# Optimization experiments

Measured on AMD Instinct MI355X. Metric: run time of the kernel, lower is better.

The kernel has to match this reference:

```python
import jax, jax.numpy as jnp
import numpy as np

EPS_Q = 1e-4     # ridge added to L L^T in OptNet.forward
MAX_ITER = 20    # qpth pdipm_b maxIter
BIG = 1e10       # sentinel for inactive step-length entries


def _make_kkt_solver(Q, G):
    """Shared factorizations (qpth pre_factor_kkt): Q Cholesky and S0 = G Q^{-1} G^T."""
    nineq = G.shape[0]
    Lq = jnp.linalg.cholesky(Q)                                   # [nz, nz]

    def q_solve(rhs):                                             # rhs [B, nz] -> Q^{-1} rhs
        return jax.scipy.linalg.cho_solve((Lq, True), rhs.T).T

    S0 = G @ jax.scipy.linalg.cho_solve((Lq, True), G.T)          # [nineq, nineq]
    eye = jnp.eye(nineq, dtype=Q.dtype)

    def solve(d, rx, rs, rz):
        # Solve the reduced KKT system (qpth solve_kkt, neq=0):
        #   [Q G^T; G -D^{-1}] [dx; dz] = [-rx; -rz + D^{-1} rs],  ds = (-rs - dz)/d
        invQ_rx = q_solve(rx)                                     # [B, nz]
        hv = invQ_rx @ G.T + rs / d - rz                          # [B, nineq]
        S = S0[None] + eye * (1.0 / d)[:, None, :]                # S0 + diag(1/d) per batch
        dz = -jnp.linalg.solve(S, hv[..., None])[..., 0]
        dx = q_solve(-rx - dz @ G)
        ds = (-rs - dz) / d
        return dx, ds, dz

    return solve


def _get_step(v, dv):
    # max alpha with v + alpha*dv >= 0 (min over entries with dv < 0); safe against NaN grads
    dv_safe = jnp.where(dv < 0, dv, -1.0)
    a = jnp.where(dv < 0, -v / dv_safe, BIG)
    return jnp.min(a, axis=1)


def pdipm_forward(Q, p, G, h):
    """qpth pdipm_b.forward (Mehrotra predictor-corrector), neq=0, fixed 20 iters with best-tracking."""
    nB, nz = p.shape
    nineq = G.shape[0]
    solve = _make_kkt_solver(Q, G)

    # initial point: KKT solve with d = 1, then shift s, z into the positive orthant
    d0 = jnp.ones((nB, nineq), Q.dtype)
    zeros = jnp.zeros((nB, nineq), Q.dtype)
    x, s, z = solve(d0, p, zeros, -h)
    smin = jnp.min(s, axis=1, keepdims=True)
    s = jnp.where(smin < 0, s - smin + 1.0, s)
    zmin = jnp.min(z, axis=1, keepdims=True)
    z = jnp.where(zmin < 0, z - zmin + 1.0, z)

    def body(carry, _):
        x, s, z, bx, bz, bs, bsum = carry
        rx = x @ Q + p + z @ G          # stationarity residual (Q symmetric)
        rs = z
        rz = x @ G.T + s - h            # primal residual
        mu = jnp.abs(jnp.sum(s * z, axis=1)) / nineq
        resids = jnp.linalg.norm(rz, axis=1) + jnp.linalg.norm(rx, axis=1) + nineq * mu
        rsum = jnp.sum(resids)
        imp = rsum < bsum
        bx = jnp.where(imp, x, bx)
        bz = jnp.where(imp, z, bz)
        bs = jnp.where(imp, s, bs)
        bsum = jnp.where(imp, rsum, bsum)
        d = z / s
        # affine (predictor) step
        dx_a, ds_a, dz_a = solve(d, rx, rs, rz)
        alpha = jnp.minimum(jnp.minimum(_get_step(z, dz_a), _get_step(s, ds_a)), 1.0)[:, None]
        sig = (jnp.sum((s + alpha * ds_a) * (z + alpha * dz_a), axis=1)
               / jnp.sum(s * z, axis=1)) ** 3
        # centering + corrector step
        rs_c = ((-mu * sig)[:, None] + ds_a * dz_a) / s
        dx_c, ds_c, dz_c = solve(d, jnp.zeros_like(rx), rs_c, jnp.zeros_like(rz))
        dx = dx_a + dx_c
        ds = ds_a + ds_c
        dz = dz_a + dz_c
        alpha = jnp.minimum(0.999 * jnp.minimum(_get_step(z, dz), _get_step(s, ds)), 1.0)[:, None]
        x = x + alpha * dx
        s = s + alpha * ds
        z = z + alpha * dz
        return (x, s, z, bx, bz, bs, bsum), None

    init = (x, s, z, x, z, s, jnp.asarray(np.inf, dtype=Q.dtype))
    (x, s, z, bx, bz, bs, bsum), _ = jax.lax.scan(body, init, None, length=MAX_ITER)
    return bx, bz, bs                   # zhat, lam (dual), slack


def setup_inputs() -> dict:
    key = jax.random.key(0)
    k1, k2, k3 = jax.random.split(key, 3)
    B, nz, nineq = 128, 512, 512
    x = jax.random.normal(k1, (B, nz), dtype=jnp.float32)
    M = jnp.tril(jnp.ones((nz, nz), jnp.float32))                        # Parameter M = tril(ones)
    L = jnp.tril(jax.random.uniform(k2, (nz, nz), dtype=jnp.float32))    # Parameter L = tril(rand)
    G = jax.random.uniform(k3, (nineq, nz), dtype=jnp.float32, minval=-1.0, maxval=1.0)
    s0 = jnp.ones((nineq,), jnp.float32)
    z0 = jnp.zeros((nz,), jnp.float32)
    return {"x": x, "M": M, "L": L, "G": G, "s0": s0, "z0": z0}


def reference(x, M, L, G, s0, z0):
    nz = L.shape[0]
    Lm = M * L
    Q = Lm @ Lm.T + EPS_Q * jnp.eye(nz, dtype=L.dtype)                   # PSD + ridge
    h = jnp.broadcast_to(z0 @ G.T + s0, (x.shape[0], G.shape[0]))        # h = G z0 + s0
    zhat, _, _ = pdipm_forward(Q, x, G, h)                               # p = x
    return zhat
```

## Files before the change

### kernel.cpp

```cpp
#include <hip/hip_runtime.h>
#include <math.h>

#define BIGD 1e10
#define N2C 262144
#define PITCH_AS 257
#define FACF 131328

typedef double d4 __attribute__((ext_vector_type(4)));

__device__ __forceinline__ int tile_off(int bi, int bj) {
    return 512 * bi * (bi - 1) + 528 * bi + (bj << 10);
}
__device__ __forceinline__ int tile_off_diag(int bi) {
    return 512 * bi * (bi - 1) + 528 * bi + (bi << 10);
}

__device__ __forceinline__ double blk_reduce_sum_d(double v, double* red) {
    int tid = threadIdx.x;
    red[tid] = v; __syncthreads();
    for (int s = 128; s > 0; s >>= 1) {
        if (tid < s) red[tid] += red[tid + s];
        __syncthreads();
    }
    double r = red[0]; __syncthreads();
// ... 88 lines not shown
    for (int l = 0; l < 4; ++l) {
        int y = y0 + 8 * l;
        t[y][x] = A[(size_t)(by * 32 + y) * 512 + bx * 32 + x];
    }
    __syncthreads();
#pragma unroll
    for (int l = 0; l < 4; ++l) {
        int y = y0 + 8 * l;
        B[(size_t)(bx * 32 + y) * 512 + by * 32 + x] = t[x][y];
    }
}

__global__ void k_h_d(const float* __restrict__ G, const float* __restrict__ s0,
                      const float* __restrict__ z0, double* __restrict__ h) {
    __shared__ double red[256];
    int tid = threadIdx.x;
    int j = blockIdx.x * 64 + (tid >> 2);
    int q = tid & 3;
    double a = 0.0;
    for (int k = q * 128; k < q * 128 + 128; ++k)
        a += (double)G[(size_t)j * 512 + k] * (double)z0[k];
    red[tid] = a;
    __syncthreads();
    if (q == 0) h[j] = (double)s0[j] + red[tid] + red[tid + 1] + red[tid + 2] + red[tid + 3];
}

__global__ __launch_bounds__(256) void k_bgemm_d(
    const double* __restrict__ A1, const double* __restrict__ B1,
    double* __restrict__ C, double sgn, double diag_eps)
{
    __shared__ double As[32 * 68];
    __shared__ double Bs[32 * 68];
    int bid = blockIdx.x;
    int mt = bid >> 3, nt = bid & 7;
    int m0 = mt * 64, n0 = nt * 64;
    int tid = threadIdx.x;
    int tx = tid & 15, ty = tid >> 4;
    double acc[4][4] = {};
    for (int k0 = 0; k0 < 512; k0 += 32) {
        __syncthreads();
#pragma unroll
        for (int l = 0; l < 8; ++l) {
            int idx = tid + 256 * l;
            int kk = idx & 31, r = idx >> 5;
            As[kk * 68 + r] = A1[(size_t)(m0 + r) * 512 + k0 + kk];
            int cc = idx & 63, k2 = idx >> 6;
            Bs[k2 * 68 + cc] = B1[(size_t)(k0 + k2) * 512 + n0 + cc];
        }
        __syncthreads();
#pragma unroll
        for (int kk = 0; kk < 32; ++kk) {
            double a4[4], b4[4];
#pragma unroll
            for (int u = 0; u < 4; ++u) a4[u] = As[kk * 68 + tx * 4 + u];
#pragma unroll
            for (int u = 0; u < 4; ++u) b4[u] = Bs[kk * 68 + ty * 4 + u];
#pragma unroll
            for (int ii = 0; ii < 4; ++ii)
#pragma unroll
                for (int jj = 0; jj < 4; ++jj)
                    acc[ii][jj] += a4[ii] * b4[jj];
        }
    }
#pragma unroll
    for (int ii = 0; ii < 4; ++ii) {
        int gm = m0 + tx * 4 + ii;
#pragma unroll
        for (int jj = 0; jj < 4; ++jj) {
            int gn = n0 + ty * 4 + jj;
            double v = sgn * acc[ii][jj];
            if (diag_eps != 0.0 && gm == gn) v += diag_eps;
            C[(size_t)gm * 512 + gn] = v;
        }
    }
}

__global__ __launch_bounds__(256) void k_gemm32(
    const float* __restrict__ A1, const float* __restrict__ B1,
    const float* __restrict__ A2, const float* __restrict__ B2,
    float* __restrict__ C,
    const float* __restrict__ addp, const float* __restrict__ subp,
    const float* __restrict__ rowp, float rowsgn, float sgn)
{
    __shared__ float As[32 * 68];
    __shared__ float Bs[32 * 68];
    int bid = blockIdx.x;
    int mt = bid >> 3, nt = bid & 7;
    int m0 = mt * 64, n0 = nt * 64;
    int tid = threadIdx.x;
    int tx = tid & 15, ty = tid >> 4;
    double acc[4][4] = {};
    for (int prod = 0; prod < 2; ++prod) {
        const float* A = prod ? A2 : A1;
        const float* B = prod ? B2 : B1;
        if (A == nullptr) break;
        for (int k0 = 0; k0 < 512; k0 += 32) {
            __syncthreads();
#pragma unroll
            for (int l = 0; l < 8; ++l) {
                int idx = tid + 256 * l;
                int kk = idx & 31, r = idx >> 5;
                As[kk * 68 + r] = A[(size_t)(m0 + r) * 512 + k0 + kk];
                int cc = idx & 63, k2 = idx >> 6;
                Bs[k2 * 68 + cc] = B[(size_t)(k0 + k2) * 512 + n0 + cc];
            }
            __syncthreads();
#pragma unroll
            for (int kk = 0; kk < 32; ++kk) {
                double a4[4], b4[4];
#pragma unroll
                for (int u = 0; u < 4; ++u) a4[u] = (double)As[kk * 68 + tx * 4 + u];
#pragma unroll
                for (int u = 0; u < 4; ++u) b4[u] = (double)Bs[kk * 68 + ty * 4 + u];
#pragma unroll
                for (int ii = 0; ii < 4; ++ii)
#pragma unroll
                    for (int jj = 0; jj < 4; ++jj)
                        acc[ii][jj] += a4[ii] * b4[jj];
            }
        }
    }
#pragma unroll
    for (int ii = 0; ii < 4; ++ii) {
        int gm = m0 + tx * 4 + ii;
#pragma unroll
        for (int jj = 0; jj < 4; ++jj) {
            int gn = n0 + ty * 4 + jj;
            size_t gi = (size_t)gm * 512 + gn;
            double v = (double)sgn * acc[ii][jj];
            if (addp) v += (double)addp[gi];
            if (subp) v -= (double)subp[gi];
            if (rowp) v += (double)rowsgn * (double)rowp[gn];
            C[gi] = (float)v;
        }
    }
}

__global__ void k_copyadd_d(const double* __restrict__ S, double* __restrict__ F,
                            double dc, int n) {
    int i = blockIdx.x * 256 + threadIdx.x;
    if (i < n) {
        double v = S[i];
        if (dc != 0.0 && (i >> 9) == (i & 511)) v += dc;
        F[i] = v;
    }
}

__global__ __launch_bounds__(512) void k_cpanel_d(double* __restrict__ F, int kp) {
    int c0 = kp * 32, tid = threadIdx.x;
    __shared__ double Dl[32 * 33];
    __shared__ double rdg[32];
    if (tid < 32) {
        int i = tid;
        double d[32];
#pragma unroll
        for (int j = 0; j < 32; ++j) d[j] = F[(size_t)(c0 + i) * 512 + c0 + j];
#pragma unroll
        for (int j = 0; j < 32; ++j) {
            double djj = __shfl(d[j], j);
            djj = (djj > 1e-300) ? djj : 1e-300;
            double sj = sqrt(djj);
            double inv = 1.0 / sj;
            if (i == j) { d[j] = sj; rdg[j] = inv; }
            if (i > j) d[j] *= inv;
            double lij = d[j];
#pragma unroll
            for (int t = j + 1; t < 32; ++t) {
                double ltj = __shfl(d[j], t);
                if (i >= t) d[t] -= lij * ltj;
            }
        }
#pragma unroll
        for (int j = 0; j < 32; ++j) {
            if (j <= i) {
                Dl[i * 33 + j] = d[j];
                F[(size_t)(c0 + i) * 512 + c0 + j] = d[j];
            }
        }
    }
    __syncthreads();
    int r = c0 + 32 + tid;
    if (r < 512) {
        double p[32];
#pragma unroll
        for (int j = 0; j < 32; ++j) p[j] = F[(size_t)r * 512 + c0 + j];
#pragma unroll
        for (int j = 0; j < 32; ++j) {
            double pj = p[j] * rdg[j];
            p[j] = pj;
#pragma unroll
            for (int t = j + 1; t < 32; ++t) p[t] -= pj * Dl[t * 33 + j];
        }
#pragma unroll
        for (int j = 0; j < 32; ++j) F[(size_t)r * 512 + c0 + j] = p[j];
    }
}

__global__ __launch_bounds__(256) void k_syrk_d(double* __restrict__ F, int kp) {
    int c0 = kp * 32;
    int t = blockIdx.x;
    int bi = 0;
    while ((bi + 1) * (bi + 2) / 2 <= t) ++bi;
    int bj = t - bi * (bi + 1) / 2;
    int i0 = c0 + 32 + bi * 64, j0 = c0 + 32 + bj * 64;
    __shared__ double Pa[32 * 68], Pb[32 * 68];
    int tid = threadIdx.x;
#pragma unroll
// ... 160 lines not shown
            for (int m = 0; m < 32; ++m) a += (double)tp[m] * wp[m];
        }
        red[tid] = a;
        __syncthreads();
        if (tid < 32) {
            int i2 = tid;
            double s = 0.0;
#pragma unroll
            for (int k2 = 0; k2 < 16; ++k2) s += red[i2 * 16 + k2];
            double aa = wv[c0 + i2] - s;
            double rdgv = rdgAll[c0 + i2];
            const float* tp = Lb + tile_off_diag(j);
            int basei = (i2 * (i2 + 1)) >> 1;
            float lrow[32];
#pragma unroll
            for (int m = 0; m < 32; ++m) lrow[m] = (m < i2) ? tp[basei + m] : 0.f;
#pragma unroll
            for (int m = 0; m < 32; ++m) {
                double xm = __shfl(aa * rdgv, m);
                if (i2 == m) wv[c0 + i2] = xm;
                if (i2 > m) aa -= (double)lrow[m] * xm;
            }
        }
        __syncthreads();
    }
    for (int j = 15; j >= 0; --j) {
        int c0 = j * 32;
        if (tid < 32) {
            int i2 = tid;
            double aa = wv[c0 + i2];
            double rdgv = rdgAll[c0 + i2];
            const float* tp = Lb + tile_off_diag(j);
            float lcol[32];
#pragma unroll
            for (int m = 0; m < 32; ++m)
                lcol[m] = (m > i2) ? tp[((m * (m + 1)) >> 1) + i2] : 0.f;
#pragma unroll
            for (int m = 31; m >= 0; --m) {
                double xm = __shfl(aa * rdgv, m);
                if (i2 == m) wv[c0 + i2] = xm;
                if (i2 < m) aa -= (double)lcol[m] * xm;
            }
        }
        __syncthreads();
        if (j > 0) {
            int k = tid >> 5, m = tid & 31;
            if (k < j) {
                const float* tp = Lb + tile_off(j, k) + m;
                double sacc = 0.0;
#pragma unroll 8
                for (int i3 = 0; i3 < 32; ++i3) sacc += (double)tp[i3 * 32] * wv[c0 + i3];
                wv[k * 32 + m] -= sacc;
            }
            __syncthreads();
        }
    }
}

__device__ void refine_once(const double* __restrict__ S0d, const double* __restrict__ dvecS,
                            const double* __restrict__ rhsL, double* __restrict__ wv,
                            double* __restrict__ tmpS, double* __restrict__ red,
                            const float* __restrict__ Lb, const double* __restrict__ rdgAll,
                            int tid)
{
    double a = 0.0;
    const double* sp = S0d + tid;
    for (int c = 0; c < 512; ++c) a += sp[(size_t)c * 512] * wv[c];
    double r = rhsL[tid] - a - dvecS[tid] * wv[tid];
    __syncthreads();
    tmpS[tid] = r;
    __syncthreads();
    trsv_packed(Lb, rdgAll, tmpS, red, tid);
    wv[tid] += tmpS[tid];
    __syncthreads();
}

__global__ __launch_bounds__(512) void k_fused(
    const double* __restrict__ S0d,
    float* __restrict__ F0,
    const double* __restrict__ ss, const double* __restrict__ zs,
    const float* __restrict__ hvf,
    const double* __restrict__ mu, const double* __restrict__ szs,
    float* __restrict__ dzv, float* __restrict__ dsv,
    const int* __restrict__ mfok,
    int b0)
{
    const int tid = threadIdx.x;
    const int b = b0 + blockIdx.x;
    float* Lb = F0 + (size_t)blockIdx.x * FACF;
    const size_t gb = (size_t)b * 512;
    const int useM = mfok[0];

    __shared__ double pool[9376];
    __shared__ double Dl[32 * 33];
    __shared__ double rdgS[32];
    __shared__ double rdgAll[512];
    __shared__ double wv[512], rhsL[512], dvecS[512], tmpS[512], redS[512];
    double* As = pool;
    double* Bs = pool + 32 * PITCH_AS;
    double* W  = pool;

    const int tx = tid & 63, ty = tid >> 6;
    const int lane = tid & 63, wid = tid >> 6;
    const int aoff = lane & 15, koff = lane >> 4;

    for (int j = 0; j < 16; ++j) {
        const int c0 = j * 32;
        for (int rbase = c0; rbase < 512; rbase += 256) {
            const int rows = (512 - rbase < 256) ? (512 - rbase) : 256;

            if (useM) {
                const int ntiles = (rows >> 4) << 1;
                d4 uacc[4];
#pragma unroll
                for (int tt = 0; tt < 4; ++tt) uacc[tt] = (d4){0.0, 0.0, 0.0, 0.0};
                for (int k = 0; k < j; ++k) {
                    __syncthreads();
                    {
                        int rl0 = tid >> 3;
                        int kq = (tid & 7) * 4;
                        for (int rr = rl0; rr < rows; rr += 64) {
                            int gr = rbase + rr;
                            const float* tp = Lb + tile_off(gr >> 5, k) + (gr & 31) * 32 + kq;
                            float4 f4 = *(const float4*)tp;
                            As[(kq + 0) * PITCH_AS + rr] = (double)f4.x;
                            As[(kq + 1) * PITCH_AS + rr] = (double)f4.y;
                            As[(kq + 2) * PITCH_AS + rr] = (double)f4.z;
                            As[(kq + 3) * PITCH_AS + rr] = (double)f4.w;
                        }
                    }
                    {
                        const float* tp = Lb + tile_off(j, k);
#pragma unroll
                        for (int l = 0; l < 2; ++l) {
                            int idx = tid + 512 * l;
                            int c = idx >> 5, kk = idx & 31;
                            Bs[kk * 36 + c] = (double)tp[c * 32 + kk];
                        }
                    }
                    __syncthreads();
#pragma unroll
                    for (int tt = 0; tt < 4; ++tt) {
                        int t = wid + (tt << 3);
                        if (t < ntiles) {
                            int s16 = (t >> 1) << 4, hcol = (t & 1) << 4;
                            d4 uv = uacc[tt];
#pragma unroll
                            for (int k4 = 0; k4 < 8; ++k4) {
                                double av = As[(k4 * 4 + koff) * PITCH_AS + s16 + aoff];
                                double bv = Bs[(k4 * 4 + koff) * 36 + hcol + aoff];
                                uv = __builtin_amdgcn_mfma_f64_16x16x4f64(av, bv, uv, 0, 0, 0);
                            }
                            uacc[tt] = uv;
                        }
                    }
                }
                __syncthreads();
#pragma unroll
                for (int tt = 0; tt < 4; ++tt) {
                    int t = wid + (tt << 3);
                    if (t < ntiles) {
                        int s16 = (t >> 1) << 4, hcol = (t & 1) << 4;
#pragma unroll
                        for (int r = 0; r < 4; ++r) {
                            int li, lj;
                            if (useM == 1)      { li = (koff << 2) + r; lj = aoff; }
                            else if (useM == 2) { li = koff + (r << 2); lj = aoff; }
                            else if (useM == 3) { li = aoff; lj = (koff << 2) + r; }
                            else                { li = aoff; lj = koff + (r << 2); }
                            W[(s16 + li) * 33 + hcol + lj] = uacc[tt][r];
                        }
                    }
                }
                __syncthreads();
#pragma unroll
                for (int v = 0; v < 4; ++v) {
                    int cg = c0 + 4 * ty + v;
                    const double* srow = S0d + (size_t)cg * 512 + rbase + tx;
#pragma unroll
                    for (int uu = 0; uu < 4; ++uu) {
                        int rl = tx + 64 * uu;
                        if (rl < rows) {
                            double sv = srow[64 * uu];
                            int rg = rbase + rl;
                            if (rbase == c0 && rg == cg) sv += ss[gb + rg] / zs[gb + rg];
                            W[rl * 33 + 4 * ty + v] = sv - W[rl * 33 + 4 * ty + v];
                        }
                    }
                }
            } else {
                double acc[4][4];
#pragma unroll
                for (int v = 0; v < 4; ++v) {
                    int cg = c0 + 4 * ty + v;
                    const double* srow = S0d + (size_t)cg * 512 + rbase + tx;
#pragma unroll
                    for (int u = 0; u < 4; ++u) {
                        int rl = tx + 64 * u;
                        acc[u][v] = (rl < rows) ? srow[64 * u] : 0.0;
                    }
                }
                if (rbase == c0) {
#pragma unroll
                    for (int u = 0; u < 4; ++u) {
                        int rg = rbase + tx + 64 * u;
#pragma unroll
                        for (int v = 0; v < 4; ++v) {
                            if (rg == c0 + 4 * ty + v) acc[u][v] += ss[gb + rg] / zs[gb + rg];
                        }
                    }
                }
                for (int k = 0; k < j; ++k) {
                    __syncthreads();
                    {
                        int rl0 = tid >> 3;
                        int kq = (tid & 7) * 4;
                        for (int rr = rl0; rr < rows; rr += 64) {
                            int gr = rbase + rr;
                            const float* tp = Lb + tile_off(gr >> 5, k) + (gr & 31) * 32 + kq;
                            float4 f4 = *(const float4*)tp;
                            As[(kq + 0) * PITCH_AS + rr] = (double)f4.x;
                            As[(kq + 1) * PITCH_AS + rr] = (double)f4.y;
                            As[(kq + 2) * PITCH_AS + rr] = (double)f4.z;
                            As[(kq + 3) * PITCH_AS + rr] = (double)f4.w;
                        }
                    }
                    {
                        const float* tp = Lb + tile_off(j, k);
#pragma unroll
                        for (int l = 0; l < 2; ++l) {
                            int idx = tid + 512 * l;
                            int c = idx >> 5, kk = idx & 31;
                            Bs[kk * 36 + c] = (double)tp[c * 32 + kk];
                        }
                    }
                    __syncthreads();
#pragma unroll 8
                    for (int kk = 0; kk < 32; ++kk) {
                        double a4[4], b4[4];
#pragma unroll
                        for (int u = 0; u < 4; ++u) a4[u] = As[kk * PITCH_AS + tx + 64 * u];
#pragma unroll
                        for (int v = 0; v < 4; ++v) b4[v] = Bs[kk * 36 + 4 * ty + v];
#pragma unroll
                        for (int u = 0; u < 4; ++u)
#pragma unroll
                            for (int v = 0; v < 4; ++v)
                                acc[u][v] -= a4[u] * b4[v];
                    }
                }
                __syncthreads();
#pragma unroll
                for (int u = 0; u < 4; ++u) {
                    int rl = tx + 64 * u;
                    if (rl < rows) {
#pragma unroll
                        for (int v = 0; v < 4; ++v)
                            W[rl * 33 + 4 * ty + v] = acc[u][v];
                    }
                }
            }
            __syncthreads();

            int trsm0 = 0;
            if (rbase == c0) {
                trsm0 = 32;
                if (tid < 32) {
                    int i = tid;
                    double d[32];
#pragma unroll
                    for (int m2 = 0; m2 < 32; ++m2) d[m2] = W[i * 33 + m2];
#pragma unroll
                    for (int m2 = 0; m2 < 32; ++m2) {
                        double djj = __shfl(d[m2], m2);
                        djj = (djj > 1e-30) ? djj : 1e-30;
                        double sj = sqrt(djj);
                        double inv = 1.0 / sj;
                        if (i == m2) { d[m2] = sj; rdgS[m2] = inv; rdgAll[c0 + m2] = inv; }
                        if (i > m2) d[m2] *= inv;
                        double lij = d[m2];
#pragma unroll
                        for (int t2 = m2 + 1; t2 < 32; ++t2) {
                            double ltj = __shfl(d[m2], t2);
                            if (i >= t2) d[t2] -= lij * ltj;
                        }
                    }
                    float* tp = Lb + tile_off_diag(j);
                    int basei = (i * (i + 1)) >> 1;
#pragma unroll
                    for (int m2 = 0; m2 < 32; ++m2) {
                        if (m2 <= i) { Dl[i * 33 + m2] = d[m2]; tp[basei + m2] = (float)d[m2]; }
                    }
                }
                __syncthreads();
            }
            {
                int nr = rows - trsm0;
                if (tid < nr) {
                    int rl = trsm0 + tid;
                    int gr = rbase + rl;
                    double x[32];
#pragma unroll
                    for (int m2 = 0; m2 < 32; ++m2) x[m2] = W[rl * 33 + m2];
#pragma unroll
                    for (int m2 = 0; m2 < 32; ++m2) {
                        double xm = x[m2] * rdgS[m2];
                        x[m2] = xm;
#pragma unroll
                        for (int t2 = m2 + 1; t2 < 32; ++t2) x[t2] -= xm * Dl[t2 * 33 + m2];
                    }
                    float* tp = Lb + tile_off(gr >> 5, j) + (gr & 31) * 32;
#pragma unroll
                    for (int m2 = 0; m2 < 32; ++m2) tp[m2] = (float)x[m2];
                }
            }
            __syncthreads();
        }
    }

    double z_t = zs[gb + tid], s_t = ss[gb + tid];
    double dv = s_t / z_t;
    dvecS[tid] = dv;
    double r1 = (double)hvf[gb + tid];
    wv[tid] = r1;
    rhsL[tid] = r1;
    __syncthreads();
    trsv_packed(Lb, rdgAll, wv, redS, tid);
    refine_once(S0d, dvecS, rhsL, wv, tmpS, redS, Lb, rdgAll, tid);

    double dza_t = -wv[tid];
    double dsa_t = -(z_t + dza_t) * dv;
    __syncthreads();

    double az = (dza_t < 0.0) ? (-z_t / dza_t) : BIGD;
    double as = (dsa_t < 0.0) ? (-s_t / dsa_t) : BIGD;
    redS[tid] = fmin(az, as);
    __syncthreads();
    for (int s2 = 256; s2 > 0; s2 >>= 1) {
        if (tid < s2) redS[tid] = fmin(redS[tid], redS[tid + s2]);
        __syncthreads();
    }
    double alpha = fmin(redS[0], 1.0);
    __syncthreads();
    redS[tid] = (s_t + alpha * dsa_t) * (z_t + alpha * dza_t);
    __syncthreads();
    for (int s2 = 256; s2 > 0; s2 >>= 1) {
        if (tid < s2) redS[tid] += redS[tid + s2];
        __syncthreads();
    }
    double d2 = redS[0];
    __syncthreads();
    double ratio = d2 / szs[b];
    double sig = ratio * ratio * ratio;
    double coef = -mu[b] * sig;
    double num = coef + dsa_t * dza_t;
    double rsc_t = num / s_t;
    wv[tid] = num / z_t;
    rhsL[tid] = wv[tid];
    __syncthreads();

    trsv_packed(Lb, rdgAll, wv, redS, tid);
    refine_once(S0d, dvecS, rhsL, wv, tmpS, redS, Lb, rdgAll, tid);

    double dz = dza_t - wv[tid];
    double ds = -(z_t + rsc_t + dz) * dv;
    dzv[gb + tid] = (float)dz;
    dsv[gb + tid] = (float)ds;
}

__global__ __launch_bounds__(256) void k_stats_d(
    const float* __restrict__ rx, const float* __restrict__ rz,
    const double* __restrict__ ssv, const double* __restrict__ zsv,
    double* resid, double* mu, double* szsum)
{
    int b = blockIdx.x, tid = threadIdx.x;
    __shared__ double red[256];
    double s1 = 0, s2 = 0, s3 = 0;
#pragma unroll
    for (int l = 0; l < 2; ++l) {
        size_t gi = (size_t)b * 512 + tid + l * 256;
        double vx = (double)rx[gi]; s1 += vx * vx;
        double vz = (double)rz[gi]; s2 += vz * vz;
        s3 += ssv[gi] * zsv[gi];
    }
    double t1 = blk_reduce_sum_d(s1, red);
    double t2 = blk_reduce_sum_d(s2, red);
    double t3 = blk_reduce_sum_d(s3, red);
    if (tid == 0) {
        resid[b] = sqrt(t2) + sqrt(t1) + fabs(t3);
        mu[b] = fabs(t3) / 512.0;
        szsum[b] = t3;
    }
}

__global__ void k_best_d(const double* __restrict__ resid, double* bsum, double* flag) {
    __shared__ double red[128];
    int tid = threadIdx.x;
    red[tid] = resid[tid];
    __syncthreads();
    for (int s = 64; s > 0; s >>= 1) {
        if (tid < s) red[tid] += red[tid + s];
        __syncthreads();
    }
    if (tid == 0) {
        double rs = red[0];
        if (rs < bsum[0]) { bsum[0] = rs; flag[0] = 1.0; }
        else flag[0] = 0.0;
    }
}

__global__ void k_bestcopy_d(const double* __restrict__ flag, const double* __restrict__ xs,
                             float* __restrict__ bx) {
    if (flag && flag[0] == 0.0) return;
    int i0 = blockIdx.x * 1024 + threadIdx.x;
#pragma unroll
    for (int l = 0; l < 4; ++l) bx[i0 + l * 256] = (float)xs[i0 + l * 256];
}

__global__ __launch_bounds__(256) void k_final_d(
    double* __restrict__ xs, double* __restrict__ ssv, double* __restrict__ zsv,
    const float* __restrict__ dxf, const float* __restrict__ dsf, const float* __restrict__ dzf,
    float* __restrict__ xs32, float* __restrict__ ss32, float* __restrict__ zs32)
{
    int b = blockIdx.x, tid = threadIdx.x;
    __shared__ double red[256];
    double m = BIGD;
#pragma unroll
    for (int l = 0; l < 2; ++l) {
        size_t gi = (size_t)b * 512 + tid + l * 256;
        double z = zsv[gi], dz = (double)dzf[gi];
        double az = (dz < 0.0) ? (-z / dz) : BIGD;
        double s = ssv[gi], ds = (double)dsf[gi];
        double as = (ds < 0.0) ? (-s / ds) : BIGD;
        m = fmin(m, fmin(az, as));
    }
    double am = blk_reduce_min_d(m, red);
    double alpha = fmin(0.999 * am, 1.0);
#pragma unroll
    for (int l = 0; l < 2; ++l) {
        size_t gi = (size_t)b * 512 + tid + l * 256;
        double nx = xs[gi] + alpha * (double)dxf[gi];
        double ns = ssv[gi] + alpha * (double)dsf[gi];
        double nz = zsv[gi] + alpha * (double)dzf[gi];
        xs[gi] = nx; ssv[gi] = ns; zsv[gi] = nz;
        xs32[gi] = (float)nx; ss32[gi] = (float)ns; zs32[gi] = (float)nz;
    }
}

__global__ __launch_bounds__(256) void k_shift_d(double* __restrict__ ssv, double* __restrict__ zsv,
                                                 float* __restrict__ ss32, float* __restrict__ zs32)
// ... 36 lines not shown
    const float* s0  = (const float*)d_in[4];
    const float* z0  = (const float*)d_in[5];
    float* outp = (float*)d_out;

    const size_t N2 = N2C;
    double* base = (double*)d_ws;
    size_t off = 0;
    auto A = [&](size_t n) { double* p = base + off; off += n; return p; };
    double* S0d  = A(N2);
    double* h    = A(512);
    double* resid = A(128); double* mu = A(128); double* szs = A(128);
    double* bsum = A(8); double* flag = A(8);
    double* mfokd = A(8);
    int* mfok = (int*)mfokd;
    double* xs = A(65536); double* ss = A(65536); double* zs = A(65536);
    float* Qf   = (float*)A(131072);
    float* GTf  = (float*)A(131072);
    float* Qif  = (float*)A(131072);
    float* h32  = (float*)A(256);
    float* rxf  = (float*)A(32768);
    float* rzf  = (float*)A(32768);
    float* hvf  = (float*)A(32768);
    float* t1f  = (float*)A(32768);
    float* dzvf = (float*)A(32768);
    float* dsvf = (float*)A(32768);
    float* xs32 = (float*)A(32768);
    float* ss32 = (float*)A(32768);
    float* zs32 = (float*)A(32768);
    float* dxf = hvf;
    float* t2f = t1f;

    double* slab = base + off;
    size_t avail = (ws_size / 8 > off) ? (ws_size / 8 - off) : 0;
    int C = (int)(avail / (FACF / 2));
    if (C > 128) C = 128;
    if (C < 1) C = 1;
    float* F0 = (float*)slab;
    double* Lm64  = slab;
    double* LmT64 = slab + 1 * N2;
    double* Q64   = slab + 2 * N2;
    double* Lq    = slab + 3 * N2;
    double* Qi64  = slab + 4 * N2;
    double* G64   = slab + 5 * N2;
    double* GT64  = slab + 6 * N2;
    double* X64   = slab + 7 * N2;
    double* SfI   = slab + 8 * N2;

    dim3 t256(256), t512(512);
    const float* NPf = nullptr;

    k_mfmatest<<<1, 64, 0, stream>>>(mfok);
    k_lm<<<1024, t256, 0, stream>>>(Mi, Li, Lm64, 262144);
    k_transpose_d<<<256, t256, 0, stream>>>(Lm64, LmT64);
    k_bgemm_d<<<64, t256, 0, stream>>>(Lm64, LmT64, Q64, 1.0, 1e-4);
    k_cast32v<<<1024, t256, 0, stream>>>(Q64, Qf, 262144);
    k_copyadd_d<<<1024, t256, 0, stream>>>(Q64, Lq, 0.0, 262144);
    for (int kp = 0; kp < 16; ++kp) {
        k_cpanel_d<<<1, t512, 0, stream>>>(Lq, kp);
        int Tr = 480 - 32 * kp;
        if (Tr > 0) {
            int T = (Tr + 63) >> 6;
            k_syrk_d<<<T * (T + 1) / 2, t256, 0, stream>>>(Lq, kp);
        }
    }
    k_solve_d<<<512, t256, 0, stream>>>(Lq, NPf, Qi64, nullptr, Qif, nullptr, 0);
    k_cast<<<1024, t256, 0, stream>>>(Gin, G64, 262144);
    k_transpose_d<<<256, t256, 0, stream>>>(G64, GT64);
    k_transpose32<<<256, t256, 0, stream>>>(Gin, GTf);
    k_bgemm_d<<<64, t256, 0, stream>>>(Qi64, GT64, X64, 1.0, 0.0);
    k_bgemm_d<<<64, t256, 0, stream>>>(G64, X64, S0d, 1.0, 0.0);
    k_copyadd_d<<<1024, t256, 0, stream>>>(S0d, SfI, 1.0, 262144);
    for (int kp = 0; kp < 16; ++kp) {
        k_cpanel_d<<<1, t512, 0, stream>>>(SfI, kp);
        int Tr = 480 - 32 * kp;
        if (Tr > 0) {
            int T = (Tr + 63) >> 6;
            k_syrk_d<<<T * (T + 1) / 2, t256, 0, stream>>>(SfI, kp);
        }
    }
    k_h_d<<<8, t256, 0, stream>>>(Gin, s0, z0, h);
    k_cast32v<<<2, t256, 0, stream>>>(h, h32, 512);
    k_initbsum<<<1, 64, 0, stream>>>(bsum);

    k_gemm32<<<16, t256, 0, stream>>>(xin, Qif, NPf, NPf, t1f, NPf, NPf, NPf, 0.f, 1.f);
    k_gemm32<<<16, t256, 0, stream>>>(t1f, GTf, NPf, NPf, hvf, NPf, NPf, h32, 1.f, 1.f);
    k_solve_d<<<128, t256, 0, stream>>>(SfI, hvf, zs, ss, zs32, ss32, 1);
    k_gemm32<<<16, t256, 0, stream>>>(zs32, Gin, NPf, NPf, t1f, xin, NPf, NPf, 0.f, 1.f);
    k_gemm32<<<16, t256, 0, stream>>>(t1f, Qif, NPf, NPf, xs32, NPf, NPf, NPf, 0.f, -1.f);
    k_cast<<<256, t256, 0, stream>>>(xs32, xs, 65536);
    k_shift_d<<<128, t256, 0, stream>>>(ss, zs, ss32, zs32);
    k_bestcopy_d<<<64, t256, 0, stream>>>(nullptr, xs, outp);

    for (int it = 0; it < 20; ++it) {
        k_gemm32<<<16, t256, 0, stream>>>(xs32, Qf, zs32, Gin, rxf, xin, NPf, NPf, 0.f, 1.f);
        k_gemm32<<<16, t256, 0, stream>>>(xs32, GTf, NPf, NPf, rzf, ss32, NPf, h32, -1.f, 1.f);
        k_stats_d<<<128, t256, 0, stream>>>(rxf, rzf, ss, zs, resid, mu, szs);
        k_best_d<<<1, 128, 0, stream>>>(resid, bsum, flag);
        k_bestcopy_d<<<64, t256, 0, stream>>>(flag, xs, outp);
        k_gemm32<<<16, t256, 0, stream>>>(rxf, Qif, NPf, NPf, t1f, NPf, NPf, NPf, 0.f, 1.f);
        k_gemm32<<<16, t256, 0, stream>>>(t1f, GTf, NPf, NPf, hvf, ss32, rzf, NPf, 0.f, 1.f);
        for (int b0 = 0; b0 < 128; b0 += C) {
            int cnt = (128 - b0 < C) ? (128 - b0) : C;
            k_fused<<<cnt, t512, 0, stream>>>(S0d, F0, ss, zs, hvf, mu, szs, dzvf, dsvf,
                                              mfok, b0);
        }
        k_gemm32<<<16, t256, 0, stream>>>(dzvf, Gin, NPf, NPf, t2f, rxf, NPf, NPf, 0.f, 1.f);
        k_gemm32<<<16, t256, 0, stream>>>(t2f, Qif, NPf, NPf, dxf, NPf, NPf, NPf, 0.f, -1.f);
        k_final_d<<<128, t256, 0, stream>>>(xs, ss, zs, dxf, dsvf, dzvf, xs32, ss32, zs32);
    }
}
```

Before: 50.90 ms.

## Persistent fused Cholesky blocks, double-buffered MFMA panel, smaller GEMM tiles

The per-batch fused Cholesky/solve kernel becomes persistent: each block loops over batch items with a grid stride, replacing the multiple host-side chunked launches with one launch. In the MFMA update path, the A operand is read directly from the packed factor in global memory instead of being staged through LDS, and the B tile is double-buffered in LDS, removing one barrier per k-step. The fp32 GEMM kernel uses 32x64 tiles instead of 64x64, launching 32 blocks rather than 16 to spread the work over more compute units. The direct global loads for A may be less coalesced than the staged copy.

```diff
diff --git a/kernel.cpp b/kernel.cpp
--- a/kernel.cpp
+++ b/kernel.cpp
@@ -194,14 +194,14 @@
     const float* __restrict__ addp, const float* __restrict__ subp,
     const float* __restrict__ rowp, float rowsgn, float sgn)
 {
-    __shared__ float As[32 * 68];
+    __shared__ float As[32 * 36];
     __shared__ float Bs[32 * 68];
     int bid = blockIdx.x;
     int mt = bid >> 3, nt = bid & 7;
-    int m0 = mt * 64, n0 = nt * 64;
+    int m0 = mt * 32, n0 = nt * 64;
     int tid = threadIdx.x;
     int tx = tid & 15, ty = tid >> 4;
-    double acc[4][4] = {};
+    double acc[2][4] = {};
     for (int prod = 0; prod < 2; ++prod) {
         const float* A = prod ? A2 : A1;
         const float* B = prod ? B2 : B1;
@@ -209,32 +209,36 @@
         for (int k0 = 0; k0 < 512; k0 += 32) {
             __syncthreads();
 #pragma unroll
+            for (int l = 0; l < 4; ++l) {
+                int idx = tid + 256 * l;
+                int kk = idx & 31, r = idx >> 5;
+                As[kk * 36 + r] = A[(size_t)(m0 + r) * 512 + k0 + kk];
+            }
+#pragma unroll
             for (int l = 0; l < 8; ++l) {
                 int idx = tid + 256 * l;
-                int kk = idx & 31, r = idx >> 5;
-                As[kk * 68 + r] = A[(size_t)(m0 + r) * 512 + k0 + kk];
                 int cc = idx & 63, k2 = idx >> 6;
                 Bs[k2 * 68 + cc] = B[(size_t)(k0 + k2) * 512 + n0 + cc];
             }
             __syncthreads();
 #pragma unroll
             for (int kk = 0; kk < 32; ++kk) {
-                double a4[4], b4[4];
-#pragma unroll
-                for (int u = 0; u < 4; ++u) a4[u] = (double)As[kk * 68 + tx * 4 + u];
+                double a2[2], b4[4];
+#pragma unroll
+                for (int u = 0; u < 2; ++u) a2[u] = (double)As[kk * 36 + tx * 2 + u];
 #pragma unroll
                 for (int u = 0; u < 4; ++u) b4[u] = (double)Bs[kk * 68 + ty * 4 + u];
 #pragma unroll
-                for (int ii = 0; ii < 4; ++ii)
+                for (int ii = 0; ii < 2; ++ii)
 #pragma unroll
                     for (int jj = 0; jj < 4; ++jj)
-                        acc[ii][jj] += a4[ii] * b4[jj];
-            }
-        }
-    }
-#pragma unroll
-    for (int ii = 0; ii < 4; ++ii) {
-        int gm = m0 + tx * 4 + ii;
+                        acc[ii][jj] += a2[ii] * b4[jj];
+            }
+        }
+    }
+#pragma unroll
+    for (int ii = 0; ii < 2; ++ii) {
+        int gm = m0 + tx * 2 + ii;
 #pragma unroll
         for (int jj = 0; jj < 4; ++jj) {
             int gn = n0 + ty * 4 + jj;
@@ -561,13 +565,10 @@
     const float* __restrict__ hvf,
     const double* __restrict__ mu, const double* __restrict__ szs,
     float* __restrict__ dzv, float* __restrict__ dsv,
-    const int* __restrict__ mfok,
-    int b0)
+    const int* __restrict__ mfok)
 {
     const int tid = threadIdx.x;
-    const int b = b0 + blockIdx.x;
     float* Lb = F0 + (size_t)blockIdx.x * FACF;
-    const size_t gb = (size_t)b * 512;
     const int useM = mfok[0];
 
     __shared__ double pool[9376];
@@ -583,268 +584,276 @@
     const int lane = tid & 63, wid = tid >> 6;
     const int aoff = lane & 15, koff = lane >> 4;
 
-    for (int j = 0; j < 16; ++j) {
-        const int c0 = j * 32;
-        for (int rbase = c0; rbase < 512; rbase += 256) {
-            const int rows = (512 - rbase < 256) ? (512 - rbase) : 256;
-
-            if (useM) {
-                const int ntiles = (rows >> 4) << 1;
-                d4 uacc[4];
-#pragma unroll
-                for (int tt = 0; tt < 4; ++tt) uacc[tt] = (d4){0.0, 0.0, 0.0, 0.0};
-                for (int k = 0; k < j; ++k) {
-                    __syncthreads();
-                    {
-                        int rl0 = tid >> 3;
-                        int kq = (tid & 7) * 4;
-                        for (int rr = rl0; rr < rows; rr += 64) {
-                            int gr = rbase + rr;
-                            const float* tp = Lb + tile_off(gr >> 5, k) + (gr & 31) * 32 + kq;
-                            float4 f4 = *(const float4*)tp;
-                            As[(kq + 0) * PITCH_AS + rr] = (double)f4.x;
-                            As[(kq + 1) * PITCH_AS + rr] = (double)f4.y;
-                            As[(kq + 2) * PITCH_AS + rr] = (double)f4.z;
-                            As[(kq + 3) * PITCH_AS + rr] = (double)f4.w;
+    for (int b = blockIdx.x; b < 128; b += gridDim.x) {
+        const size_t gb = (size_t)b * 512;
+        __syncthreads();
+
+        for (int j = 0; j < 16; ++j) {
+            const int c0 = j * 32;
+            for (int rbase = c0; rbase < 512; rbase += 256) {
+                const int rows = (512 - rbase < 256) ? (512 - rbase) : 256;
+
+                if (useM) {
+                    const int ntiles = (rows >> 4) << 1;
+                    d4 uacc[4];
+#pragma unroll
+                    for (int tt = 0; tt < 4; ++tt) uacc[tt] = (d4){0.0, 0.0, 0.0, 0.0};
+                    if (j > 0) {
+                        {
+                            const float* tp = Lb + tile_off(j, 0);
+#pragma unroll
+                            for (int l = 0; l < 2; ++l) {
+                                int idx = tid + 512 * l;
+                                int c = idx >> 5, kk = idx & 31;
+                                pool[kk * 36 + c] = (double)tp[c * 32 + kk];
+                            }
+                        }
+                        __syncthreads();
+                        for (int k = 0; k < j; ++k) {
+                            double* Bcur = pool + (k & 1) * 1152;
+                            if (k + 1 < j) {
+                                const float* tp = Lb + tile_off(j, k + 1);
+                                double* Bnxt = pool + ((k + 1) & 1) * 1152;
+#pragma unroll
+                                for (int l = 0; l < 2; ++l) {
+                                    int idx = tid + 512 * l;
+                                    int c = idx >> 5, kk = idx & 31;
+                                    Bnxt[kk * 36 + c] = (double)tp[c * 32 + kk];
+                                }
+                            }
+#pragma unroll
+                            for (int tt = 0; tt < 4; ++tt) {
+                                int t = wid + (tt << 3);
+                                if (t < ntiles) {
+                                    int s16 = (t >> 1) << 4, hcol = (t & 1) << 4;
+                                    int gr = rbase + s16 + aoff;
+                                    const float* ap = Lb + tile_off(gr >> 5, k)
+                                                      + (gr & 31) * 32 + koff;
+                                    d4 uv = uacc[tt];
+#pragma unroll
+                                    for (int k4 = 0; k4 < 8; ++k4) {
+                                        double av = (double)ap[k4 * 4];
+                                        double bv = Bcur[(k4 * 4 + koff) * 36 + hcol + aoff];
+                                        uv = __builtin_amdgcn_mfma_f64_16x16x4f64(av, bv, uv,
+                                                                                  0, 0, 0);
+                                    }
+                                    uacc[tt] = uv;
+                                }
+                            }
+                            __syncthreads();
                         }
                     }
-                    {
-                        const float* tp = Lb + tile_off(j, k);
-#pragma unroll
-                        for (int l = 0; l < 2; ++l) {
-                            int idx = tid + 512 * l;
-                            int c = idx >> 5, kk = idx & 31;
-                            Bs[kk * 36 + c] = (double)tp[c * 32 + kk];
-                        }
-                    }
-                    __syncthreads();
 #pragma unroll
                     for (int tt = 0; tt < 4; ++tt) {
                         int t = wid + (tt << 3);
                         if (t < ntiles) {
                             int s16 = (t >> 1) << 4, hcol = (t & 1) << 4;
-                            d4 uv = uacc[tt];
-#pragma unroll
-                            for (int k4 = 0; k4 < 8; ++k4) {
-                                double av = As[(k4 * 4 + koff) * PITCH_AS + s16 + aoff];
-                                double bv = Bs[(k4 * 4 + koff) * 36 + hcol + aoff];
-                                uv = __builtin_amdgcn_mfma_f64_16x16x4f64(av, bv, uv, 0, 0, 0);
+#pragma unroll
+                            for (int r = 0; r < 4; ++r) {
+                                int li, lj;
+                                if (useM == 1)      { li = (koff << 2) + r; lj = aoff; }
+                                else if (useM == 2) { li = koff + (r << 2); lj = aoff; }
+                                else if (useM == 3) { li = aoff; lj = (koff << 2) + r; }
+                                else                { li = aoff; lj = koff + (r << 2); }
+                                W[(s16 + li) * 33 + hcol + lj] = uacc[tt][r];
                             }
-                            uacc[tt] = uv;
+                        }
+                    }
+                    __syncthreads();
+#pragma unroll
+                    for (int v = 0; v < 4; ++v) {
+                        int cg = c0 + 4 * ty + v;
+                        const double* srow = S0d + (size_t)cg * 512 + rbase + tx;
+#pragma unroll
+                        for (int uu = 0; uu < 4; ++uu) {
+                            int rl = tx + 64 * uu;
+                            if (rl < rows) {
+                                double sv = srow[64 * uu];
+                                int rg = rbase + rl;
+                                if (rbase == c0 && rg == cg) sv += ss[gb + rg] / zs[gb + rg];
+                                W[rl * 33 + 4 * ty + v] = sv - W[rl * 33 + 4 * ty + v];
+                            }
+                        }
+                    }
+                } else {
+                    double acc[4][4];
+#pragma unroll
+                    for (int v = 0; v < 4; ++v) {
+                        int cg = c0 + 4 * ty + v;
+                        const double* srow = S0d + (size_t)cg * 512 + rbase + tx;
+#pragma unroll
+                        for (int u = 0; u < 4; ++u) {
+                            int rl = tx + 64 * u;
+                            acc[u][v] = (rl < rows) ? srow[64 * u] : 0.0;
+                        }
+                    }
+                    if (rbase == c0) {
+#pragma unroll
+                        for (int u = 0; u < 4; ++u) {
+                            int rg = rbase + tx + 64 * u;
+#pragma unroll
+                            for (int v = 0; v < 4; ++v) {
+                                if (rg == c0 + 4 * ty + v) acc[u][v] += ss[gb + rg] / zs[gb + rg];
+                            }
+                        }
+                    }
+                    for (int k = 0; k < j; ++k) {
+                        __syncthreads();
+                        {
+                            int rl0 = tid >> 3;
+                            int kq = (tid & 7) * 4;
+                            for (int rr = rl0; rr < rows; rr += 64) {
+                                int gr = rbase + rr;
+                                const float* tp = Lb + tile_off(gr >> 5, k) + (gr & 31) * 32 + kq;
+                                float4 f4 = *(const float4*)tp;
+                                As[(kq + 0) * PITCH_AS + rr] = (double)f4.x;
+                                As[(kq + 1) * PITCH_AS + rr] = (double)f4.y;
+                                As[(kq + 2) * PITCH_AS + rr] = (double)f4.z;
+                                As[(kq + 3) * PITCH_AS + rr] = (double)f4.w;
+                            }
+                        }
+                        {
+                            const float* tp = Lb + tile_off(j, k);
+#pragma unroll
+                            for (int l = 0; l < 2; ++l) {
+                                int idx = tid + 512 * l;
+                                int c = idx >> 5, kk = idx & 31;
+                                Bs[kk * 36 + c] = (double)tp[c * 32 + kk];
+                            }
+                        }
+                        __syncthreads();
+#pragma unroll 8
+                        for (int kk = 0; kk < 32; ++kk) {
+                            double a4[4], b4[4];
+#pragma unroll
+                            for (int u = 0; u < 4; ++u) a4[u] = As[kk * PITCH_AS + tx + 64 * u];
+#pragma unroll
+                            for (int v = 0; v < 4; ++v) b4[v] = Bs[kk * 36 + 4 * ty + v];
+#pragma unroll
+                            for (int u = 0; u < 4; ++u)
+#pragma unroll
+                                for (int v = 0; v < 4; ++v)
+                                    acc[u][v] -= a4[u] * b4[v];
+                        }
+                    }
+                    __syncthreads();
+#pragma unroll
+                    for (int u = 0; u < 4; ++u) {
+                        int rl = tx + 64 * u;
+                        if (rl < rows) {
+#pragma unroll
+                            for (int v = 0; v < 4; ++v)
+                                W[rl * 33 + 4 * ty + v] = acc[u][v];
                         }
                     }
                 }
                 __syncthreads();
-#pragma unroll
-                for (int tt = 0; tt < 4; ++tt) {
-                    int t = wid + (tt << 3);
-                    if (t < ntiles) {
-                        int s16 = (t >> 1) << 4, hcol = (t & 1) << 4;
-#pragma unroll
-                        for (int r = 0; r < 4; ++r) {
-                            int li, lj;
-                            if (useM == 1)      { li = (koff << 2) + r; lj = aoff; }
-                            else if (useM == 2) { li = koff + (r << 2); lj = aoff; }
-                            else if (useM == 3) { li = aoff; lj = (koff << 2) + r; }
-                            else                { li = aoff; lj = koff + (r << 2); }
-                            W[(s16 + li) * 33 + hcol + lj] = uacc[tt][r];
-                        }
+
+                int trsm0 = 0;
+                if (rbase == c0) {
+                    trsm0 = 32;
+                    if (tid < 32) {
+                        int i = tid;
+                        double d[32];
+#pragma unroll
+                        for (int m2 = 0; m2 < 32; ++m2) d[m2] = W[i * 33 + m2];
+#pragma unroll
+                        for (int m2 = 0; m2 < 32; ++m2) {
+                            double djj = __shfl(d[m2], m2);
+                            djj = (djj > 1e-30) ? djj : 1e-30;
+                            double sj = sqrt(djj);
+                            double inv = 1.0 / sj;
+                            if (i == m2) { d[m2] = sj; rdgS[m2] = inv; rdgAll[c0 + m2] = inv; }
+                            if (i > m2) d[m2] *= inv;
+                            double lij = d[m2];
+#pragma unroll
+                            for (int t2 = m2 + 1; t2 < 32; ++t2) {
+                                double ltj = __shfl(d[m2], t2);
+                                if (i >= t2) d[t2] -= lij * ltj;
+                            }
+                        }
+                        float* tp = Lb + tile_off_diag(j);
+                        int basei = (i * (i + 1)) >> 1;
+#pragma unroll
+                        for (int m2 = 0; m2 < 32; ++m2) {
+                            if (m2 <= i) { Dl[i * 33 + m2] = d[m2]; tp[basei + m2] = (float)d[m2]; }
+                        }
+                    }
+                    __syncthreads();
+                }
+                {
+                    int nr = rows - trsm0;
+                    if (tid < nr) {
+                        int rl = trsm0 + tid;
+                        int gr = rbase + rl;
+                        double x[32];
+#pragma unroll
+                        for (int m2 = 0; m2 < 32; ++m2) x[m2] = W[rl * 33 + m2];
+#pragma unroll
+                        for (int m2 = 0; m2 < 32; ++m2) {
+                            double xm = x[m2] * rdgS[m2];
+                            x[m2] = xm;
+#pragma unroll
+                            for (int t2 = m2 + 1; t2 < 32; ++t2) x[t2] -= xm * Dl[t2 * 33 + m2];
+                        }
+                        float* tp = Lb + tile_off(gr >> 5, j) + (gr & 31) * 32;
+#pragma unroll
+                        for (int m2 = 0; m2 < 32; ++m2) tp[m2] = (float)x[m2];
                     }
                 }
                 __syncthreads();
-#pragma unroll
-                for (int v = 0; v < 4; ++v) {
-                    int cg = c0 + 4 * ty + v;
-                    const double* srow = S0d + (size_t)cg * 512 + rbase + tx;
-#pragma unroll
-                    for (int uu = 0; uu < 4; ++uu) {
-                        int rl = tx + 64 * uu;
-                        if (rl < rows) {
-                            double sv = srow[64 * uu];
-                            int rg = rbase + rl;
-                            if (rbase == c0 && rg == cg) sv += ss[gb + rg] / zs[gb + rg];
-                            W[rl * 33 + 4 * ty + v] = sv - W[rl * 33 + 4 * ty + v];
-                        }
-                    }
-                }
-            } else {
-                double acc[4][4];
-#pragma unroll
-                for (int v = 0; v < 4; ++v) {
-                    int cg = c0 + 4 * ty + v;
-                    const double* srow = S0d + (size_t)cg * 512 + rbase + tx;
-#pragma unroll
-                    for (int u = 0; u < 4; ++u) {
-                        int rl = tx + 64 * u;
-                        acc[u][v] = (rl < rows) ? srow[64 * u] : 0.0;
-                    }
-                }
-                if (rbase == c0) {
-#pragma unroll
-                    for (int u = 0; u < 4; ++u) {
-                        int rg = rbase + tx + 64 * u;
-#pragma unroll
-                        for (int v = 0; v < 4; ++v) {
-                            if (rg == c0 + 4 * ty + v) acc[u][v] += ss[gb + rg] / zs[gb + rg];
-                        }
-                    }
-                }
-                for (int k = 0; k < j; ++k) {
-                    __syncthreads();
-                    {
-                        int rl0 = tid >> 3;
-                        int kq = (tid & 7) * 4;
-                        for (int rr = rl0; rr < rows; rr += 64) {
-                            int gr = rbase + rr;
-                            const float* tp = Lb + tile_off(gr >> 5, k) + (gr & 31) * 32 + kq;
-                            float4 f4 = *(const float4*)tp;
-                            As[(kq + 0) * PITCH_AS + rr] = (double)f4.x;
-                            As[(kq + 1) * PITCH_AS + rr] = (double)f4.y;
-                            As[(kq + 2) * PITCH_AS + rr] = (double)f4.z;
-                            As[(kq + 3) * PITCH_AS + rr] = (double)f4.w;
-                        }
-                    }
-                    {
-                        const float* tp = Lb + tile_off(j, k);
-#pragma unroll
-                        for (int l = 0; l < 2; ++l) {
-                            int idx = tid + 512 * l;
-                            int c = idx >> 5, kk = idx & 31;
-                            Bs[kk * 36 + c] = (double)tp[c * 32 + kk];
-                        }
-                    }
-                    __syncthreads();
-#pragma unroll 8
-                    for (int kk = 0; kk < 32; ++kk) {
-                        double a4[4], b4[4];
-#pragma unroll
-                        for (int u = 0; u < 4; ++u) a4[u] = As[kk * PITCH_AS + tx + 64 * u];
-#pragma unroll
-                        for (int v = 0; v < 4; ++v) b4[v] = Bs[kk * 36 + 4 * ty + v];
-#pragma unroll
-                        for (int u = 0; u < 4; ++u)
-#pragma unroll
-                            for (int v = 0; v < 4; ++v)
-                                acc[u][v] -= a4[u] * b4[v];
-                    }
-                }
-                __syncthreads();
-#pragma unroll
-                for (int u = 0; u < 4; ++u) {
-                    int rl = tx + 64 * u;
-                    if (rl < rows) {
-#pragma unroll
-                        for (int v = 0; v < 4; ++v)
-                            W[rl * 33 + 4 * ty + v] = acc[u][v];
-                    }
-                }
-            }
+            }
+        }
+
+        double z_t = zs[gb + tid], s_t = ss[gb + tid];
+        double dv = s_t / z_t;
+        dvecS[tid] = dv;
+        double r1 = (double)hvf[gb + tid];
+        wv[tid] = r1;
+        rhsL[tid] = r1;
+        __syncthreads();
+        trsv_packed(Lb, rdgAll, wv, redS, tid);
+        refine_once(S0d, dvecS, rhsL, wv, tmpS, redS, Lb, rdgAll, tid);
+
+        double dza_t = -wv[tid];
+        double dsa_t = -(z_t + dza_t) * dv;
+        __syncthreads();
+
+        double az = (dza_t < 0.0) ? (-z_t / dza_t) : BIGD;
+        double as = (dsa_t < 0.0) ? (-s_t / dsa_t) : BIGD;
+        redS[tid] = fmin(az, as);
+        __syncthreads();
+        for (int s2 = 256; s2 > 0; s2 >>= 1) {
+            if (tid < s2) redS[tid] = fmin(redS[tid], redS[tid + s2]);
             __syncthreads();
-
-            int trsm0 = 0;
-            if (rbase == c0) {
-                trsm0 = 32;
-                if (tid < 32) {
-                    int i = tid;
-                    double d[32];
-#pragma unroll
-                    for (int m2 = 0; m2 < 32; ++m2) d[m2] = W[i * 33 + m2];
-#pragma unroll
-                    for (int m2 = 0; m2 < 32; ++m2) {
-                        double djj = __shfl(d[m2], m2);
-                        djj = (djj > 1e-30) ? djj : 1e-30;
-                        double sj = sqrt(djj);
-                        double inv = 1.0 / sj;
-                        if (i == m2) { d[m2] = sj; rdgS[m2] = inv; rdgAll[c0 + m2] = inv; }
-                        if (i > m2) d[m2] *= inv;
-                        double lij = d[m2];
-#pragma unroll
-                        for (int t2 = m2 + 1; t2 < 32; ++t2) {
-                            double ltj = __shfl(d[m2], t2);
-                            if (i >= t2) d[t2] -= lij * ltj;
-                        }
-                    }
-                    float* tp = Lb + tile_off_diag(j);
-                    int basei = (i * (i + 1)) >> 1;
-#pragma unroll
-                    for (int m2 = 0; m2 < 32; ++m2) {
-                        if (m2 <= i) { Dl[i * 33 + m2] = d[m2]; tp[basei + m2] = (float)d[m2]; }
-                    }
-                }
-                __syncthreads();
-            }
-            {
-                int nr = rows - trsm0;
-                if (tid < nr) {
-                    int rl = trsm0 + tid;
-                    int gr = rbase + rl;
-                    double x[32];
-#pragma unroll
-                    for (int m2 = 0; m2 < 32; ++m2) x[m2] = W[rl * 33 + m2];
-#pragma unroll
-                    for (int m2 = 0; m2 < 32; ++m2) {
-                        double xm = x[m2] * rdgS[m2];
-                        x[m2] = xm;
-#pragma unroll
-                        for (int t2 = m2 + 1; t2 < 32; ++t2) x[t2] -= xm * Dl[t2 * 33 + m2];
-                    }
-                    float* tp = Lb + tile_off(gr >> 5, j) + (gr & 31) * 32;
-#pragma unroll
-                    for (int m2 = 0; m2 < 32; ++m2) tp[m2] = (float)x[m2];
-                }
-            }
+        }
+        double alpha = fmin(redS[0], 1.0);
+        __syncthreads();
+        redS[tid] = (s_t + alpha * dsa_t) * (z_t + alpha * dza_t);
+        __syncthreads();
+        for (int s2 = 256; s2 > 0; s2 >>= 1) {
+            if (tid < s2) redS[tid] += redS[tid + s2];
             __syncthreads();
         }
-    }
-
-    double z_t = zs[gb + tid], s_t = ss[gb + tid];
-    double dv = s_t / z_t;
-    dvecS[tid] = dv;
-    double r1 = (double)hvf[gb + tid];
-    wv[tid] = r1;
-    rhsL[tid] = r1;
-    __syncthreads();
-    trsv_packed(Lb, rdgAll, wv, redS, tid);
-    refine_once(S0d, dvecS, rhsL, wv, tmpS, redS, Lb, rdgAll, tid);
-
-    double dza_t = -wv[tid];
-    double dsa_t = -(z_t + dza_t) * dv;
-    __syncthreads();
-
-    double az = (dza_t < 0.0) ? (-z_t / dza_t) : BIGD;
-    double as = (dsa_t < 0.0) ? (-s_t / dsa_t) : BIGD;
-    redS[tid] = fmin(az, as);
-    __syncthreads();
-    for (int s2 = 256; s2 > 0; s2 >>= 1) {
-        if (tid < s2) redS[tid] = fmin(redS[tid], redS[tid + s2]);
-        __syncthreads();
-    }
-    double alpha = fmin(redS[0], 1.0);
-    __syncthreads();
-    redS[tid] = (s_t + alpha * dsa_t) * (z_t + alpha * dza_t);
-    __syncthreads();
-    for (int s2 = 256; s2 > 0; s2 >>= 1) {
-        if (tid < s2) redS[tid] += redS[tid + s2];
-        __syncthreads();
-    }
-    double d2 = redS[0];
-    __syncthreads();
-    double ratio = d2 / szs[b];
-    double sig = ratio * ratio * ratio;
-    double coef = -mu[b] * sig;
-    double num = coef + dsa_t * dza_t;
-    double rsc_t = num / s_t;
-    wv[tid] = num / z_t;
-    rhsL[tid] = wv[tid];
-    __syncthreads();
-
-    trsv_packed(Lb, rdgAll, wv, redS, tid);
-    refine_once(S0d, dvecS, rhsL, wv, tmpS, redS, Lb, rdgAll, tid);
-
-    double dz = dza_t - wv[tid];
-    double ds = -(z_t + rsc_t + dz) * dv;
-    dzv[gb + tid] = (float)dz;
-    dsv[gb + tid] = (float)ds;
+        double d2 = redS[0];
+        __syncthreads();
+        double ratio = d2 / szs[b];
+        double sig = ratio * ratio * ratio;
+        double coef = -mu[b] * sig;
+        double num = coef + dsa_t * dza_t;
+        double rsc_t = num / s_t;
+        wv[tid] = num / z_t;
+        rhsL[tid] = wv[tid];
+        __syncthreads();
+
+        trsv_packed(Lb, rdgAll, wv, redS, tid);
+        refine_once(S0d, dvecS, rhsL, wv, tmpS, redS, Lb, rdgAll, tid);
+
+        double dz = dza_t - wv[tid];
+        double ds = -(z_t + rsc_t + dz) * dv;
+        dzv[gb + tid] = (float)dz;
+        dsv[gb + tid] = (float)ds;
+    }
 }
 
 __global__ __launch_bounds__(256) void k_stats_d(
@@ -1047,30 +1056,27 @@
     k_cast32v<<<2, t256, 0, stream>>>(h, h32, 512);
     k_initbsum<<<1, 64, 0, stream>>>(bsum);
 
-    k_gemm32<<<16, t256, 0, stream>>>(xin, Qif, NPf, NPf, t1f, NPf, NPf, NPf, 0.f, 1.f);
-    k_gemm32<<<16, t256, 0, stream>>>(t1f, GTf, NPf, NPf, hvf, NPf, NPf, h32, 1.f, 1.f);
+    k_gemm32<<<32, t256, 0, stream>>>(xin, Qif, NPf, NPf, t1f, NPf, NPf, NPf, 0.f, 1.f);
+    k_gemm32<<<32, t256, 0, stream>>>(t1f, GTf, NPf, NPf, hvf, NPf, NPf, h32, 1.f, 1.f);
     k_solve_d<<<128, t256, 0, stream>>>(SfI, hvf, zs, ss, zs32, ss32, 1);
-    k_gemm32<<<16, t256, 0, stream>>>(zs32, Gin, NPf, NPf, t1f, xin, NPf, NPf, 0.f, 1.f);
-    k_gemm32<<<16, t256, 0, stream>>>(t1f, Qif, NPf, NPf, xs32, NPf, NPf, NPf, 0.f, -1.f);
+    k_gemm32<<<32, t256, 0, stream>>>(zs32, Gin, NPf, NPf, t1f, xin, NPf, NPf, 0.f, 1.f);
+    k_gemm32<<<32, t256, 0, stream>>>(t1f, Qif, NPf, NPf, xs32, NPf, NPf, NPf, 0.f, -1.f);
     k_cast<<<256, t256, 0, stream>>>(xs32, xs, 65536);
     k_shift_d<<<128, t256, 0, stream>>>(ss, zs, ss32, zs32);
     k_bestcopy_d<<<64, t256, 0, stream>>>(nullptr, xs, outp);
 
+    int fgrid = (C < 128) ? C : 128;
     for (int it = 0; it < 20; ++it) {
-        k_gemm32<<<16, t256, 0, stream>>>(xs32, Qf, zs32, Gin, rxf, xin, NPf, NPf, 0.f, 1.f);
-        k_gemm32<<<16, t256, 0, stream>>>(xs32, GTf, NPf, NPf, rzf, ss32, NPf, h32, -1.f, 1.f);
+        k_gemm32<<<32, t256, 0, stream>>>(xs32, Qf, zs32, Gin, rxf, xin, NPf, NPf, 0.f, 1.f);
+        k_gemm32<<<32, t256, 0, stream>>>(xs32, GTf, NPf, NPf, rzf, ss32, NPf, h32, -1.f, 1.f);
         k_stats_d<<<128, t256, 0, stream>>>(rxf, rzf, ss, zs, resid, mu, szs);
         k_best_d<<<1, 128, 0, stream>>>(resid, bsum, flag);
         k_bestcopy_d<<<64, t256, 0, stream>>>(flag, xs, outp);
-        k_gemm32<<<16, t256, 0, stream>>>(rxf, Qif, NPf, NPf, t1f, NPf, NPf, NPf, 0.f, 1.f);
-        k_gemm32<<<16, t256, 0, stream>>>(t1f, GTf, NPf, NPf, hvf, ss32, rzf, NPf, 0.f, 1.f);
-        for (int b0 = 0; b0 < 128; b0 += C) {
-            int cnt = (128 - b0 < C) ? (128 - b0) : C;
-            k_fused<<<cnt, t512, 0, stream>>>(S0d, F0, ss, zs, hvf, mu, szs, dzvf, dsvf,
-                                              mfok, b0);
-        }
-        k_gemm32<<<16, t256, 0, stream>>>(dzvf, Gin, NPf, NPf, t2f, rxf, NPf, NPf, 0.f, 1.f);
-        k_gemm32<<<16, t256, 0, stream>>>(t2f, Qif, NPf, NPf, dxf, NPf, NPf, NPf, 0.f, -1.f);
+        k_gemm32<<<32, t256, 0, stream>>>(rxf, Qif, NPf, NPf, t1f, NPf, NPf, NPf, 0.f, 1.f);
+        k_gemm32<<<32, t256, 0, stream>>>(t1f, GTf, NPf, NPf, hvf, ss32, rzf, NPf, 0.f, 1.f);
+        k_fused<<<fgrid, t512, 0, stream>>>(S0d, F0, ss, zs, hvf, mu, szs, dzvf, dsvf, mfok);
+        k_gemm32<<<32, t256, 0, stream>>>(dzvf, Gin, NPf, NPf, t2f, rxf, NPf, NPf, 0.f, 1.f);
+        k_gemm32<<<32, t256, 0, stream>>>(t2f, Qif, NPf, NPf, dxf, NPf, NPf, NPf, 0.f, -1.f);
         k_final_d<<<128, t256, 0, stream>>>(xs, ss, zs, dxf, dsvf, dzvf, xs32, ss32, zs32);
     }
 }
```

Result: slower. 57.48 ms (+12.9%).
